# Optimization experiments

Hardware: AMD Instinct MI355X
Metric: run time of the kernel (lower is better)

The kernel has to match this reference:

```python
import jax, jax.numpy as jnp
import numpy as np

D_MODEL = 512


def setup_inputs() -> dict:
    key = jax.random.key(0)
    ks = jax.random.split(key, 9)
    B, S, D = 2, 4096, D_MODEL
    scale = 1.0 / np.sqrt(D)
    return {
        "Q": jax.random.normal(ks[0], (B, S, D), dtype=jnp.float32),
        "K": jax.random.normal(ks[1], (B, S, D), dtype=jnp.float32),
        "V": jax.random.normal(ks[2], (B, S, D), dtype=jnp.float32),
        "W_q": jax.random.normal(ks[3], (D, D), dtype=jnp.float32) * scale,
        "b_q": jax.random.normal(ks[4], (D,), dtype=jnp.float32) * scale,
        "W_k": jax.random.normal(ks[5], (D, D), dtype=jnp.float32) * scale,
        "b_k": jax.random.normal(ks[6], (D,), dtype=jnp.float32) * scale,
        "W_v": jax.random.normal(ks[7], (D, D), dtype=jnp.float32) * scale,
        "b_v": jax.random.normal(ks[8], (D,), dtype=jnp.float32) * scale,
    }


def reference(Q, K, V, W_q, b_q, W_k, b_k, W_v, b_v):
    # Linear projections (torch Linear: x @ W.T + b)
    q = jnp.einsum("bsd,ed->bse", Q, W_q) + b_q  # [B,S,D]
    k = jnp.einsum("bsd,ed->bse", K, W_k) + b_k
    v = jnp.einsum("bsd,ed->bse", V, W_v) + b_v
    d_k = k.shape[-1]
    scores = jnp.einsum("bqd,bkd->bqk", q, k) / jnp.sqrt(jnp.asarray(d_k, q.dtype))
    attn = jax.nn.softmax(scores, axis=-1)  # [B,S,S]
    return jnp.einsum("bqk,bkd->bqd", attn, v)
```

## Files before the change

### kernel.cpp

```cpp
#include <hip/hip_runtime.h>
#include <hip/hip_bf16.h>
#include <math.h>
#include <stdint.h>

typedef __attribute__((ext_vector_type(8))) short short8;
typedef __attribute__((ext_vector_type(4))) float floatx4;
typedef __attribute__((ext_vector_type(4))) unsigned short ushort4v;

__device__ __forceinline__ void gload_lds16(const void* g, void* lds) {
    __builtin_amdgcn_global_load_lds(
        (__attribute__((address_space(1))) void*)(g),
        (__attribute__((address_space(3))) void*)(lds), 16, 0, 0);
}
__device__ __forceinline__ float bf16bits_to_f(unsigned short u) {
    union { unsigned int i; float f; } x; x.i = ((unsigned int)u) << 16; return x.f;
}
__device__ __forceinline__ unsigned short f_to_bf16bits(float f) {
    union { float f; unsigned int i; } x; x.f = f;
    unsigned int lsb = (x.i >> 16) & 1u;
    x.i += 0x7fffu + lsb;
    return (unsigned short)(x.i >> 16);
}

__global__ __launch_bounds__(256) void conv_qkv_kernel(
    const float* __restrict__ Q, const float* __restrict__ K, const float* __restrict__ V,
    unsigned short* __restrict__ out)
{
    const int seg = blockIdx.x >> 12;
    const int blk = blockIdx.x & 4095;
    const float* src = (seg == 0) ? Q : (seg == 1) ? K : V;
    const int idx = (blk * 256 + threadIdx.x) * 4;
    float4 v = *(const float4*)&src[idx];
    ushort4v o;
    o[0] = f_to_bf16bits(v.x); o[1] = f_to_bf16bits(v.y);
    o[2] = f_to_bf16bits(v.z); o[3] = f_to_bf16bits(v.w);
    *(ushort4v*)&out[(size_t)seg * 4194304 + idx] = o;
}

__global__ __launch_bounds__(256) void conv1_kernel(
    const float* __restrict__ in, unsigned short* __restrict__ out)
{
    const int idx = (blockIdx.x * 256 + threadIdx.x) * 4;
    float4 v = *(const float4*)&in[idx];
    ushort4v o;
    o[0] = f_to_bf16bits(v.x); o[1] = f_to_bf16bits(v.y);
    o[2] = f_to_bf16bits(v.z); o[3] = f_to_bf16bits(v.w);
    *(ushort4v*)&out[idx] = o;
}

__global__ __launch_bounds__(256) void conv_wb_kernel(
    const float* __restrict__ Wq, const float* __restrict__ Wk, const float* __restrict__ Wv,
    const float* __restrict__ bq, const float* __restrict__ bk, const float* __restrict__ bv,
    unsigned short* __restrict__ Wo,
    unsigned short* __restrict__ bo)
{
    const int m = blockIdx.y;
    const float* W = (m == 0) ? Wq : (m == 1) ? Wk : Wv;
    const float* b = (m == 0) ? bq : (m == 1) ? bk : bv;
    if (blockIdx.x < 256) {
        const int idx = (blockIdx.x * 256 + threadIdx.x) * 4;
        float4 v = *(const float4*)&W[idx];
        ushort4v o;
        o[0] = f_to_bf16bits(v.x); o[1] = f_to_bf16bits(v.y);
        o[2] = f_to_bf16bits(v.z); o[3] = f_to_bf16bits(v.w);
        *(ushort4v*)&Wo[(size_t)m * 262144 + idx] = o;
    } else if (threadIdx.x < 128) {
        const int idx = threadIdx.x * 4;
        float4 v = *(const float4*)&b[idx];
        ushort4v o;
        o[0] = f_to_bf16bits(v.x); o[1] = f_to_bf16bits(v.y);
        o[2] = f_to_bf16bits(v.z); o[3] = f_to_bf16bits(v.w);
        *(ushort4v*)&bo[(size_t)m * 512 + idx] = o;
    }
}

__global__ __launch_bounds__(256, 2) void proj_kernel(
    const unsigned short* __restrict__ Xall,
    size_t xstride, int mode_base,
    const unsigned short* __restrict__ Wall,
    const unsigned short* __restrict__ ball,
    unsigned short* __restrict__ qbuf,
    unsigned short* __restrict__ kbuf,
    unsigned short* __restrict__ vTbuf,
    float qscale)
{
    __shared__ __align__(16) unsigned short Xs[128 * 64];
    __shared__ __align__(16) unsigned short Ws[128 * 64];

    const int mode = mode_base + blockIdx.y;
    const unsigned short* X = Xall + (size_t)blockIdx.y * xstride;
    const unsigned short* W = Wall + (size_t)mode * 262144;
    const unsigned short* bias = ball + (size_t)mode * 512;

    const int tid = threadIdx.x;
    const int wave = tid >> 6, lane = tid & 63, quad = lane >> 4, l15 = lane & 15;
    const int m0 = (int)(blockIdx.x >> 2) << 7;
    const int n0 = (int)(blockIdx.x & 3) << 7;
    const int mw = (wave >> 1) << 6, nw = (wave & 1) << 6;

    floatx4 acc[4][4];
    #pragma unroll
    for (int i = 0; i < 4; i++)
        #pragma unroll
        for (int j = 0; j < 4; j++) acc[i][j] = floatx4{0.f, 0.f, 0.f, 0.f};

    for (int kt = 0; kt < 512; kt += 64) {
        #pragma unroll
        for (int i = 0; i < 4; i++) {
            const int r0 = wave * 32 + i * 8;
            gload_lds16(X + (size_t)(m0 + r0 + (lane >> 3)) * 512 + kt + (lane & 7) * 8, &Xs[r0 * 64]);
            gload_lds16(W + (size_t)(n0 + r0 + (lane >> 3)) * 512 + kt + (lane & 7) * 8, &Ws[r0 * 64]);
        }
        __syncthreads();
        #pragma unroll
        for (int kk = 0; kk < 64; kk += 32) {
            short8 a[4], b[4];
            #pragma unroll
            for (int i = 0; i < 4; i++) a[i] = *(const short8*)&Xs[(mw + 16 * i + l15) * 64 + kk + quad * 8];
            #pragma unroll
            for (int j = 0; j < 4; j++) b[j] = *(const short8*)&Ws[(nw + 16 * j + l15) * 64 + kk + quad * 8];
            #pragma unroll
            for (int i = 0; i < 4; i++)
                #pragma unroll
                for (int j = 0; j < 4; j++)
                    acc[i][j] = __builtin_amdgcn_mfma_f32_16x16x32_bf16(a[i], b[j], acc[i][j], 0, 0, 0);
        }
        __syncthreads();
    }

    float bfj[4];
    #pragma unroll
    for (int j = 0; j < 4; j++) bfj[j] = bf16bits_to_f(bias[n0 + nw + 16 * j + l15]);

    if (mode < 2) {
        unsigned short* out = (mode == 0) ? qbuf : kbuf;
        const float s = (mode == 0) ? qscale : 1.0f;
        #pragma unroll
        for (int i = 0; i < 4; i++) {
            const int mrow = m0 + mw + 16 * i + quad * 4;
            #pragma unroll
            for (int j = 0; j < 4; j++) {
                const int n = n0 + nw + 16 * j + l15;
                #pragma unroll
                for (int r = 0; r < 4; r++)
                    out[(size_t)(mrow + r) * 512 + n] = f_to_bf16bits((acc[i][j][r] + bfj[j]) * s);
            }
        }
    } else {
        #pragma unroll
        for (int i = 0; i < 4; i++) {
            const int mrow = m0 + mw + 16 * i + quad * 4;
            const int bb = mrow >> 12;
            const int s4 = mrow & 4095;
            #pragma unroll
            for (int j = 0; j < 4; j++) {
                const int n = n0 + nw + 16 * j + l15;
                ushort4v pk;
                #pragma unroll
                for (int r = 0; r < 4; r++) pk[r] = f_to_bf16bits(acc[i][j][r] + bfj[j]);
                *(ushort4v*)&vTbuf[((size_t)bb * 512 + n) * 4096 + s4] = pk;
            }
        }
    }
}

template <int NSPLIT>
__global__ __launch_bounds__(256, 2) void attn_kernel(
    const unsigned short* __restrict__ q,
    const unsigned short* __restrict__ k,
    const unsigned short* __restrict__ vT,
    unsigned short* __restrict__ num,
    float* __restrict__ denom)
{
    constexpr int TK  = 32;
    constexpr int KST = 520;
    constexpr int PST = 40;
    __shared__ __align__(16) unsigned short Ks[TK * KST];
    __shared__ __align__(16) unsigned short Ps[64 * PST];

    const int tid = threadIdx.x;
    const int wave = tid >> 6, lane = tid & 63, quad = lane >> 4, l15 = lane & 15;
    const int bid = blockIdx.x;
    const int sp   = bid & (NSPLIT - 1);
    const int qblk = bid / NSPLIT;
    const int bb = qblk >> 6;
    const int q0 = (qblk & 63) << 6;
    const size_t rowbase = (size_t)bb * 4096 + q0;

    short8 qf[16];
    {
        const unsigned short* qrow = q + (rowbase + 16 * wave + l15) * 512;
        #pragma unroll
        for (int t = 0; t < 16; t++) qf[t] = *(const short8*)&qrow[t * 32 + quad * 8];
    }

    floatx4 oacc[4][8];
    #pragma unroll
    for (int i = 0; i < 4; i++)
        #pragma unroll
        for (int c = 0; c < 8; c++) oacc[i][c] = floatx4{0.f, 0.f, 0.f, 0.f};
    float dsum[4] = {0.f, 0.f, 0.f, 0.f};

    const unsigned short* kb = k  + (size_t)bb * 4096 * 512;
    const unsigned short* vrow = vT + (size_t)bb * 512 * 4096
                               + (size_t)(128 * wave + l15) * 4096 + quad * 8;

    const int jbeg = sp * (4096 / NSPLIT);
    const int jend = jbeg + (4096 / NSPLIT);
    for (int j0 = jbeg; j0 < jend; j0 += TK) {
        #pragma unroll
        for (int r = 0; r < 8; r++) {
            const int row = wave * 8 + r;
            gload_lds16(kb + (size_t)(j0 + row) * 512 + lane * 8, &Ks[row * KST]);
        }
        __syncthreads();

        short8 vf[8];
        #pragma unroll
        for (int c = 0; c < 8; c++)
            vf[c] = *(const short8*)&vrow[(size_t)c * 16 * 4096 + j0];

        floatx4 sA[2], sB[2];
        sA[0] = sA[1] = sB[0] = sB[1] = floatx4{0.f, 0.f, 0.f, 0.f};
        #pragma unroll
        for (int t = 0; t < 16; t += 2) {
            #pragma unroll
            for (int c = 0; c < 2; c++) {
                short8 b0 = *(const short8*)&Ks[(c * 16 + l15) * KST + t * 32 + quad * 8];
                sA[c] = __builtin_amdgcn_mfma_f32_16x16x32_bf16(qf[t], b0, sA[c], 0, 0, 0);
                short8 b1 = *(const short8*)&Ks[(c * 16 + l15) * KST + (t + 1) * 32 + quad * 8];
                sB[c] = __builtin_amdgcn_mfma_f32_16x16x32_bf16(qf[t + 1], b1, sB[c], 0, 0, 0);
            }
        }
        #pragma unroll
        for (int c = 0; c < 2; c++) {
            #pragma unroll
            for (int r = 0; r < 4; r++) {
                const float p = __expf(fminf(sA[c][r] + sB[c][r], 30.0f));
                const unsigned short pb = f_to_bf16bits(p);
                dsum[r] += bf16bits_to_f(pb);
                Ps[(16 * wave + quad * 4 + r) * PST + c * 16 + l15] = pb;
            }
        }
        __syncthreads();

        short8 ap[4];
        #pragma unroll
        for (int i = 0; i < 4; i++) ap[i] = *(const short8*)&Ps[(16 * i + l15) * PST + quad * 8];
        #pragma unroll
        for (int c = 0; c < 8; c++) {
            #pragma unroll
            for (int i = 0; i < 4; i++)
                oacc[i][c] = __builtin_amdgcn_mfma_f32_16x16x32_bf16(ap[i], vf[c], oacc[i][c], 0, 0, 0);
        }
    }

    #pragma unroll
    for (int r = 0; r < 4; r++) {
        float v = dsum[r];
        v += __shfl_xor(v, 1);
        v += __shfl_xor(v, 2);
        v += __shfl_xor(v, 4);
        v += __shfl_xor(v, 8);
        dsum[r] = v;
    }
    if (l15 == 0) {
        #pragma unroll
        for (int r = 0; r < 4; r++)
            denom[(size_t)sp * 8192 + rowbase + 16 * wave + quad * 4 + r] = dsum[r];
    }

    #pragma unroll
    for (int i = 0; i < 4; i++) {
        #pragma unroll
        for (int r = 0; r < 4; r++) {
            const size_t row = rowbase + 16 * i + quad * 4 + r;
            unsigned short* np_ = num + ((size_t)sp * 8192 + row) * 512 + 128 * wave + l15;
            #pragma unroll
            for (int c = 0; c < 8; c++)
                np_[16 * c] = f_to_bf16bits(oacc[i][c][r]);
        }
    }
}

__global__ __launch_bounds__(256) void combine_kernel(
    const unsigned short* __restrict__ num,
    const float* __restrict__ denom,
    float* __restrict__ out,
    int nsplit)
{
    const int gid = blockIdx.x * 256 + threadIdx.x;
    const int srow = gid >> 6;
    const int d0 = (gid & 63) << 3;
    float s[8];
    #pragma unroll
    for (int e = 0; e < 8; e++) s[e] = 0.f;
    float den = 0.f;
    for (int sp = 0; sp < nsplit; sp++) {
        den += denom[(size_t)sp * 8192 + srow];
        short8 v = *(const short8*)(num + ((size_t)sp * 8192 + srow) * 512 + d0);
        #pragma unroll
        for (int e = 0; e < 8; e++) s[e] += bf16bits_to_f((unsigned short)v[e]);
    }
    const float inv = 1.0f / den;
    float4 o0, o1;
    o0.x = s[0] * inv; o0.y = s[1] * inv; o0.z = s[2] * inv; o0.w = s[3] * inv;
    o1.x = s[4] * inv; o1.y = s[5] * inv; o1.z = s[6] * inv; o1.w = s[7] * inv;
    float* op = out + (size_t)srow * 512 + d0;
    *(float4*)op = o0;
    *(float4*)(op + 4) = o1;
}

extern "C" void kernel_launch(void* const* d_in, const int* in_sizes, int n_in,
                              void* d_out, int out_size, void* d_ws, size_t ws_size,
                              hipStream_t stream)
{
    (void)in_sizes; (void)n_in; (void)out_size;
    const float* Qin = (const float*)d_in[0];
    const float* Kin = (const float*)d_in[1];
    const float* Vin = (const float*)d_in[2];
    const float* Wq  = (const float*)d_in[3];
    const float* bq  = (const float*)d_in[4];
    const float* Wk  = (const float*)d_in[5];
    const float* bk  = (const float*)d_in[6];
    const float* Wv  = (const float*)d_in[7];
    const float* bv  = (const float*)d_in[8];

    const size_t M   = (size_t)8192 * 512;
    const size_t WS_ = (size_t)512 * 512;

    auto need = [&](size_t sa, int ns) -> size_t {
        return (sa + 3 * M) * 2 + 3 * WS_ * 2 + 3 * 512 * 2 + 64 + (size_t)ns * 8192 * 4;
    };
    int nsplit; size_t sa; bool batched;
    if      (ws_size >= need(8 * M, 8)) { nsplit = 8; sa = 8 * M; batched = true; }
    else if (ws_size >= need(4 * M, 4)) { nsplit = 4; sa = 4 * M; batched = true; }
    else if (ws_size >= need(3 * M, 2)) { nsplit = 2; sa = 3 * M; batched = true; }
    else                                { nsplit = 1; sa = 1 * M; batched = false; }

    unsigned short* ws    = (unsigned short*)d_ws;
    unsigned short* slotA = ws;
    unsigned short* qs    = ws + sa;
    unsigned short* ks    = qs + M;
    unsigned short* vT    = ks + M;
    unsigned short* Wc    = vT + M;
    unsigned short* bc    = Wc + 3 * WS_;
    float* denom = (float*)(((uintptr_t)(bc + 3 * 512) + 15) & ~(uintptr_t)15);
    unsigned short* numb = slotA;

    const float qscale = 1.0f / sqrtf(512.0f);

    conv_wb_kernel<<<dim3(257, 3), dim3(256), 0, stream>>>(Wq, Wk, Wv, bq, bk, bv, Wc, bc);

    if (batched) {
        conv_qkv_kernel<<<dim3(3 * 4096), dim3(256), 0, stream>>>(Qin, Kin, Vin, slotA);
        proj_kernel<<<dim3(256, 3), dim3(256), 0, stream>>>(
            slotA, M, 0, Wc, bc, qs, ks, vT, qscale);
    } else {
        const float* Xin[3] = { Qin, Kin, Vin };
        for (int m = 0; m < 3; m++) {
            conv1_kernel<<<dim3(4096), dim3(256), 0, stream>>>(Xin[m], slotA);
            proj_kernel<<<dim3(256, 1), dim3(256), 0, stream>>>(
                slotA, 0, m, Wc, bc, qs, ks, vT, qscale);
        }
    }

    if (nsplit == 8)
        attn_kernel<8><<<dim3(1024), dim3(256), 0, stream>>>(qs, ks, vT, numb, denom);
    else if (nsplit == 4)
        attn_kernel<4><<<dim3(512), dim3(256), 0, stream>>>(qs, ks, vT, numb, denom);
    else if (nsplit == 2)
        attn_kernel<2><<<dim3(256), dim3(256), 0, stream>>>(qs, ks, vT, numb, denom);
    else
        attn_kernel<1><<<dim3(128), dim3(256), 0, stream>>>(qs, ks, vT, numb, denom);

    combine_kernel<<<dim3(2048), dim3(256), 0, stream>>>(
        numb, denom, (float*)d_out, nsplit);
}
```

Measured before the change: 259.9 us.

## Tile V layout for contiguous loads, fuse conversions, vectorize num stores, cap split at four

The transposed V buffer is stored in 16x8 tiles, so each lane's per-chunk V fragment load reads one contiguous 128-bit line instead of striding across 4096-element rows. The attention numerator is written as packed 8-wide vectors in a permuted column order, and the combine kernel undoes that permutation with strided scalar fp32 stores. The weight/bias and Q/K/V conversion kernels are merged into one launch, and the 8-way key split is dropped so at most 4 splits are used. Fewer splits shrink the partial-sum traffic but launch half as many attention blocks, which may leave compute units underused.

After: 224.9 us. -13.5%, faster.

```diff
diff --git a/kernel.cpp b/kernel.cpp
--- a/kernel.cpp
+++ b/kernel.cpp
@@ -22,19 +22,38 @@
     return (unsigned short)(x.i >> 16);
 }
 
-__global__ __launch_bounds__(256) void conv_qkv_kernel(
+__global__ __launch_bounds__(256) void conv_all_kernel(
     const float* __restrict__ Q, const float* __restrict__ K, const float* __restrict__ V,
-    unsigned short* __restrict__ out)
-{
-    const int seg = blockIdx.x >> 12;
-    const int blk = blockIdx.x & 4095;
-    const float* src = (seg == 0) ? Q : (seg == 1) ? K : V;
-    const int idx = (blk * 256 + threadIdx.x) * 4;
+    const float* __restrict__ Wq, const float* __restrict__ Wk, const float* __restrict__ Wv,
+    const float* __restrict__ bq, const float* __restrict__ bk, const float* __restrict__ bv,
+    unsigned short* __restrict__ qkv,
+    unsigned short* __restrict__ Wo,
+    unsigned short* __restrict__ bo)
+{
+    const int gid = blockIdx.x;
+    const float* src; unsigned short* dst; int idx;
+    if (gid < 12288) {
+        const int seg = gid >> 12, blk = gid & 4095;
+        src = (seg == 0) ? Q : (seg == 1) ? K : V;
+        dst = qkv + (size_t)seg * 4194304;
+        idx = (blk * 256 + threadIdx.x) * 4;
+    } else if (gid < 13056) {
+        const int t = gid - 12288, m = t >> 8, blk = t & 255;
+        src = (m == 0) ? Wq : (m == 1) ? Wk : Wv;
+        dst = Wo + (size_t)m * 262144;
+        idx = (blk * 256 + threadIdx.x) * 4;
+    } else {
+        const int m = gid - 13056;
+        if (threadIdx.x >= 128) return;
+        src = (m == 0) ? bq : (m == 1) ? bk : bv;
+        dst = bo + (size_t)m * 512;
+        idx = threadIdx.x * 4;
+    }
     float4 v = *(const float4*)&src[idx];
     ushort4v o;
     o[0] = f_to_bf16bits(v.x); o[1] = f_to_bf16bits(v.y);
     o[2] = f_to_bf16bits(v.z); o[3] = f_to_bf16bits(v.w);
-    *(ushort4v*)&out[(size_t)seg * 4194304 + idx] = o;
+    *(ushort4v*)&dst[idx] = o;
 }
 
 __global__ __launch_bounds__(256) void conv1_kernel(
@@ -51,8 +70,7 @@
 __global__ __launch_bounds__(256) void conv_wb_kernel(
     const float* __restrict__ Wq, const float* __restrict__ Wk, const float* __restrict__ Wv,
     const float* __restrict__ bq, const float* __restrict__ bk, const float* __restrict__ bv,
-    unsigned short* __restrict__ Wo,
-    unsigned short* __restrict__ bo)
+    unsigned short* __restrict__ Wo, unsigned short* __restrict__ bo)
 {
     const int m = blockIdx.y;
     const float* W = (m == 0) ? Wq : (m == 1) ? Wk : Wv;
@@ -151,14 +169,15 @@
         for (int i = 0; i < 4; i++) {
             const int mrow = m0 + mw + 16 * i + quad * 4;
             const int bb = mrow >> 12;
-            const int s4 = mrow & 4095;
+            const int k4 = mrow & 4095;
+            const size_t kpart = (size_t)bb * 2097152 + (size_t)(k4 >> 3) * 128 + (k4 & 7);
             #pragma unroll
             for (int j = 0; j < 4; j++) {
                 const int n = n0 + nw + 16 * j + l15;
                 ushort4v pk;
                 #pragma unroll
                 for (int r = 0; r < 4; r++) pk[r] = f_to_bf16bits(acc[i][j][r] + bfj[j]);
-                *(ushort4v*)&vTbuf[((size_t)bb * 512 + n) * 4096 + s4] = pk;
+                *(ushort4v*)&vTbuf[kpart + (size_t)(n >> 4) * 65536 + (n & 15) * 8] = pk;
             }
         }
     }
@@ -201,9 +220,9 @@
         for (int c = 0; c < 8; c++) oacc[i][c] = floatx4{0.f, 0.f, 0.f, 0.f};
     float dsum[4] = {0.f, 0.f, 0.f, 0.f};
 
-    const unsigned short* kb = k  + (size_t)bb * 4096 * 512;
-    const unsigned short* vrow = vT + (size_t)bb * 512 * 4096
-                               + (size_t)(128 * wave + l15) * 4096 + quad * 8;
+    const unsigned short* kb = k + (size_t)bb * 4096 * 512;
+    const unsigned short* vbase = vT + (size_t)bb * 2097152
+                                + (size_t)(8 * wave) * 65536 + quad * 128 + l15 * 8;
 
     const int jbeg = sp * (4096 / NSPLIT);
     const int jend = jbeg + (4096 / NSPLIT);
@@ -218,7 +237,7 @@
         short8 vf[8];
         #pragma unroll
         for (int c = 0; c < 8; c++)
-            vf[c] = *(const short8*)&vrow[(size_t)c * 16 * 4096 + j0];
+            vf[c] = *(const short8*)&vbase[(size_t)c * 65536 + (j0 << 4)];
 
         floatx4 sA[2], sB[2];
         sA[0] = sA[1] = sB[0] = sB[1] = floatx4{0.f, 0.f, 0.f, 0.f};
@@ -275,10 +294,10 @@
         #pragma unroll
         for (int r = 0; r < 4; r++) {
             const size_t row = rowbase + 16 * i + quad * 4 + r;
-            unsigned short* np_ = num + ((size_t)sp * 8192 + row) * 512 + 128 * wave + l15;
-            #pragma unroll
-            for (int c = 0; c < 8; c++)
-                np_[16 * c] = f_to_bf16bits(oacc[i][c][r]);
+            short8 pk;
+            #pragma unroll
+            for (int c = 0; c < 8; c++) pk[c] = (short)f_to_bf16bits(oacc[i][c][r]);
+            *(short8*)&num[((size_t)sp * 8192 + row) * 512 + wave * 128 + l15 * 8] = pk;
         }
     }
 }
@@ -291,24 +310,22 @@
 {
     const int gid = blockIdx.x * 256 + threadIdx.x;
     const int srow = gid >> 6;
-    const int d0 = (gid & 63) << 3;
+    const int sub = gid & 63;
+    const int w = sub >> 4, l15 = sub & 15;
     float s[8];
     #pragma unroll
     for (int e = 0; e < 8; e++) s[e] = 0.f;
     float den = 0.f;
     for (int sp = 0; sp < nsplit; sp++) {
         den += denom[(size_t)sp * 8192 + srow];
-        short8 v = *(const short8*)(num + ((size_t)sp * 8192 + srow) * 512 + d0);
+        short8 v = *(const short8*)(num + ((size_t)sp * 8192 + srow) * 512 + w * 128 + l15 * 8);
         #pragma unroll
         for (int e = 0; e < 8; e++) s[e] += bf16bits_to_f((unsigned short)v[e]);
     }
     const float inv = 1.0f / den;
-    float4 o0, o1;
-    o0.x = s[0] * inv; o0.y = s[1] * inv; o0.z = s[2] * inv; o0.w = s[3] * inv;
-    o1.x = s[4] * inv; o1.y = s[5] * inv; o1.z = s[6] * inv; o1.w = s[7] * inv;
-    float* op = out + (size_t)srow * 512 + d0;
-    *(float4*)op = o0;
-    *(float4*)(op + 4) = o1;
+    float* op = out + (size_t)srow * 512 + w * 128 + l15;
+    #pragma unroll
+    for (int c = 0; c < 8; c++) op[16 * c] = s[c] * inv;
 }
 
 extern "C" void kernel_launch(void* const* d_in, const int* in_sizes, int n_in,
@@ -333,8 +350,7 @@
         return (sa + 3 * M) * 2 + 3 * WS_ * 2 + 3 * 512 * 2 + 64 + (size_t)ns * 8192 * 4;
     };
     int nsplit; size_t sa; bool batched;
-    if      (ws_size >= need(8 * M, 8)) { nsplit = 8; sa = 8 * M; batched = true; }
-    else if (ws_size >= need(4 * M, 4)) { nsplit = 4; sa = 4 * M; batched = true; }
+    if      (ws_size >= need(4 * M, 4)) { nsplit = 4; sa = 4 * M; batched = true; }
     else if (ws_size >= need(3 * M, 2)) { nsplit = 2; sa = 3 * M; batched = true; }
     else                                { nsplit = 1; sa = 1 * M; batched = false; }
 
@@ -350,13 +366,13 @@
 
     const float qscale = 1.0f / sqrtf(512.0f);
 
-    conv_wb_kernel<<<dim3(257, 3), dim3(256), 0, stream>>>(Wq, Wk, Wv, bq, bk, bv, Wc, bc);
-
     if (batched) {
-        conv_qkv_kernel<<<dim3(3 * 4096), dim3(256), 0, stream>>>(Qin, Kin, Vin, slotA);
+        conv_all_kernel<<<dim3(13059), dim3(256), 0, stream>>>(
+            Qin, Kin, Vin, Wq, Wk, Wv, bq, bk, bv, slotA, Wc, bc);
         proj_kernel<<<dim3(256, 3), dim3(256), 0, stream>>>(
             slotA, M, 0, Wc, bc, qs, ks, vT, qscale);
     } else {
+        conv_wb_kernel<<<dim3(257, 3), dim3(256), 0, stream>>>(Wq, Wk, Wv, bq, bk, bv, Wc, bc);
         const float* Xin[3] = { Qin, Kin, Vin };
         for (int m = 0; m < 3; m++) {
             conv1_kernel<<<dim3(4096), dim3(256), 0, stream>>>(Xin[m], slotA);
@@ -365,9 +381,7 @@
         }
     }
 
-    if (nsplit == 8)
-        attn_kernel<8><<<dim3(1024), dim3(256), 0, stream>>>(qs, ks, vT, numb, denom);
-    else if (nsplit == 4)
+    if (nsplit == 4)
         attn_kernel<4><<<dim3(512), dim3(256), 0, stream>>>(qs, ks, vT, numb, denom);
     else if (nsplit == 2)
         attn_kernel<2><<<dim3(256), dim3(256), 0, stream>>>(qs, ks, vT, numb, denom);
```
